# Performance work log

Hardware: AMD Instinct MI355X
Metric: run time of the kernel (lower is better)

## Reference

```python
import jax, jax.numpy as jnp
import numpy as np

B, N, D = 8, 2048, 512  # batch, input_dim (tokens), weight_dim


def setup_inputs() -> dict:
    key = jax.random.key(0)
    ks = jax.random.split(key, 7)
    return {
        "query": jax.random.normal(ks[0], (B, N, D), dtype=jnp.float32),
        "key": jax.random.normal(ks[1], (B, N, D), dtype=jnp.float32),
        "value": jax.random.normal(ks[2], (B, N, D), dtype=jnp.float32),
        "W_query": jax.random.normal(ks[3], (D, D), dtype=jnp.float32),
        "W_key": jax.random.normal(ks[4], (D, D), dtype=jnp.float32),
        "W_value": jax.random.normal(ks[5], (D, D), dtype=jnp.float32),
        "self_importance": jnp.zeros((N,), dtype=jnp.float32),
    }


def reference(query, key, value, W_query, W_key, W_value, self_importance):
    d = W_query.shape[0]
    q = jnp.einsum("bnd,de->bne", query, W_query)
    k = jnp.einsum("bnd,de->bne", key, W_key)
    v = jnp.einsum("bnd,de->bne", value, W_value)
    scores = jnp.einsum("bqe,bke->bqk", q, k) / jnp.sqrt(jnp.float32(d))
    # diagonal self-importance bias: eye(N) * clamp(exp(s), max=3)
    importance = jnp.minimum(jnp.exp(self_importance), 3.0)  # [N]
    n = scores.shape[1]
    idx = jnp.arange(n)
    scores = scores.at[:, idx, idx].add(importance)
    attn = jax.nn.softmax(scores, axis=-1)  # [B, N, N]
    entropy_loss = -jnp.mean(jnp.sum(attn * jnp.log(attn + 1e-10), axis=-1))
    out = jnp.einsum("bqk,bke->bqe", attn, v)
    return (out, attn, entropy_loss)
```

## Files before the change

### kernel.cpp

```cpp
#include <hip/hip_runtime.h>
#include <math.h>

#define BB 8
#define NN 2048
#define DD 512

typedef _Float16 halfT;
typedef _Float16 half8 __attribute__((ext_vector_type(8)));
typedef _Float16 half4 __attribute__((ext_vector_type(4)));
typedef float f32x4 __attribute__((ext_vector_type(4)));

#define GLOAD16(gp, sp) __builtin_amdgcn_global_load_lds( \
    (const __attribute__((address_space(1))) void*)(gp), \
    (__attribute__((address_space(3))) void*)(sp), 16, 0, 0)

__global__ __launch_bounds__(256) void wsplit_kernel(
    const float* __restrict__ Wq, const float* __restrict__ Wk, const float* __restrict__ Wv,
    _Float16* __restrict__ qhT, _Float16* __restrict__ qlT,
    _Float16* __restrict__ khT, _Float16* __restrict__ klT,
    _Float16* __restrict__ vhT)
{
    __shared__ float t[64][65];
    const int z = blockIdx.z;
    const float* W = (z == 0) ? Wq : ((z == 1) ? Wk : Wv);
    _Float16* Ph = (z == 0) ? qhT : ((z == 1) ? khT : vhT);
    _Float16* Pl = (z == 0) ? qlT : ((z == 1) ? klT : nullptr);
    const int bx = blockIdx.x * 64, by = blockIdx.y * 64;
    const int tid = threadIdx.x;
    #pragma unroll
    for (int i = 0; i < 16; ++i) {
        const int idx = i * 256 + tid;
        const int r = idx >> 6, c = idx & 63;
        t[r][c] = W[(long)(by + r) * 512 + bx + c];
    }
    __syncthreads();
    #pragma unroll
    for (int i = 0; i < 16; ++i) {
        const int idx = i * 256 + tid;
        const int r = idx >> 6, c = idx & 63;
        const float v = t[c][r];
        const _Float16 h = (_Float16)v;
        const long o = (long)(bx + r) * 512 + by + c;
        Ph[o] = h;
        if (z < 2) Pl[o] = (_Float16)(v - (float)h);
    }
}

__global__ __launch_bounds__(512, 2) void proj_kernel(
    const float* __restrict__ X0, const float* __restrict__ X1, const float* __restrict__ X2,
    const halfT* __restrict__ B0h, const halfT* __restrict__ B0l,
    const halfT* __restrict__ B1h, const halfT* __restrict__ B1l,
    const halfT* __restrict__ B2h,
    halfT* __restrict__ O0h, halfT* __restrict__ O0l,
    halfT* __restrict__ O1h, halfT* __restrict__ O1l,
    halfT* __restrict__ O2)
{
    extern __shared__ __align__(16) char smem[];

    const int tid  = threadIdx.x;
    const int lane = tid & 63;
    const int w    = tid >> 6;
    const int wr   = w >> 1, wc = w & 1;

    const int h = blockIdx.x;
    int z, nx, my;
    if (h < 512) {
        const int L = ((h & 7) << 6) | (h >> 3);
        z = L >> 8; nx = L & 3; my = (L >> 2) & 63;
    } else {
        const int hv = h - 512;
        const int L = ((hv & 7) << 5) | (hv >> 3);
        z = 2; nx = L & 3; my = L >> 2;
    }
    const int bm = my * 256, bn = nx * 128;
    const bool full = (z < 2);

    const float* X = (z == 0) ? X0 : ((z == 1) ? X1 : X2);
    const halfT* Bgh = (z == 0) ? B0h : ((z == 1) ? B1h : B2h);
    const halfT* Bgl = (z == 0) ? B0l : B1l;
    halfT* Oh = (z == 0) ? O0h : O1h;
    halfT* Ol = (z == 0) ? O0l : O1l;

    const int b_row   = w * 16 + (lane >> 2);
    const int b_chunk = (lane & 3) ^ ((lane >> 3) & 3);
    const long gB = (long)(bn + b_row) * DD + b_chunk * 8;
    const int ldstB = w * 1024;

    const int a_row0 = tid >> 2;
    const int a_gc   = tid & 3;
    const int a_phys = a_gc ^ ((a_row0 >> 1) & 3);
    const long gA0 = (long)(bm + a_row0) * DD + a_gc * 8;
    const long gA1 = (long)(bm + a_row0 + 128) * DD + a_gc * 8;
    const int aOff0 = a_row0 * 64 + a_phys * 16;
    const int aOff1 = (a_row0 + 128) * 64 + a_phys * 16;

    float ar[16];
    auto loadA = [&](int t) {
        const long kk = (long)t * 32;
        *(float4*)&ar[0]  = *(const float4*)(X + gA0 + kk);
        *(float4*)&ar[4]  = *(const float4*)(X + gA0 + kk + 4);
        *(float4*)&ar[8]  = *(const float4*)(X + gA1 + kk);
        *(float4*)&ar[12] = *(const float4*)(X + gA1 + kk + 4);
    };
    auto stageB = [&](char* buf, int t) {
        const long kk = (long)t * 32;
        GLOAD16(Bgh + gB + kk, buf + 32768 + ldstB);
        if (full) GLOAD16(Bgl + gB + kk, buf + 40960 + ldstB);
    };
    auto writeA = [&](char* buf) {
        half8 h0, l0, h1, l1;
        #pragma unroll
        for (int i = 0; i < 8; ++i) {
            const _Float16 hh = (_Float16)ar[i];
            h0[i] = hh; l0[i] = (_Float16)(ar[i] - (float)hh);
        }
        #pragma unroll
        for (int i = 0; i < 8; ++i) {
            const _Float16 hh = (_Float16)ar[8 + i];
            h1[i] = hh; l1[i] = (_Float16)(ar[8 + i] - (float)hh);
        }
        *(half8*)(buf + aOff0) = h0;
        *(half8*)(buf + aOff1) = h1;
        if (full) {
            *(half8*)(buf + 16384 + aOff0) = l0;
            *(half8*)(buf + 16384 + aOff1) = l1;
        }
    };

    const int lr  = lane & 15;
    const int q16 = lane >> 4;
    const int frag = lr * 64 + ((q16 ^ ((lr >> 1) & 3)) << 4);
    const int abase = wr * 4096 + frag;
    const int bbase = wc * 4096 + frag;

    f32x4 acc[4][4];
    #pragma unroll
    for (int i = 0; i < 4; ++i)
        #pragma unroll
        for (int j = 0; j < 4; ++j) acc[i][j] = (f32x4)0.0f;

    loadA(0);
    stageB(smem, 0);
    writeA(smem);
    asm volatile("s_waitcnt vmcnt(0) lgkmcnt(0)" ::: "memory");
    __builtin_amdgcn_s_barrier();
    __builtin_amdgcn_sched_barrier(0);

    for (int t = 0; t < 16; ++t) {
        char* cur = smem + (size_t)(t & 1) * 49152;
        char* nxt = smem + (size_t)((t + 1) & 1) * 49152;
        const bool pf = (t < 15);

        if (pf) { loadA(t + 1); stageB(nxt, t + 1); }

        half8 ah[4], bh[4], bl[4];
        #pragma unroll
        for (int m = 0; m < 4; ++m)
            ah[m] = *(const half8*)(cur + abase + m * 1024);
        #pragma unroll
        for (int j = 0; j < 4; ++j)
            bh[j] = *(const half8*)(cur + 32768 + bbase + j * 1024);
        __builtin_amdgcn_s_setprio(1);
        #pragma unroll
        for (int m = 0; m < 4; ++m)
            #pragma unroll
            for (int j = 0; j < 4; ++j)
                acc[m][j] = __builtin_amdgcn_mfma_f32_16x16x32_f16(ah[m], bh[j], acc[m][j], 0, 0, 0);
        __builtin_amdgcn_s_setprio(0);

        if (full) {
            #pragma unroll
            for (int j = 0; j < 4; ++j)
                bl[j] = *(const half8*)(cur + 40960 + bbase + j * 1024);
            __builtin_amdgcn_s_setprio(1);
            #pragma unroll
            for (int m = 0; m < 4; ++m)
                #pragma unroll
                for (int j = 0; j < 4; ++j)
                    acc[m][j] = __builtin_amdgcn_mfma_f32_16x16x32_f16(ah[m], bl[j], acc[m][j], 0, 0, 0);
            __builtin_amdgcn_s_setprio(0);

            __builtin_amdgcn_s_setprio(1);
            #pragma unroll
            for (int m = 0; m < 4; ++m) {
                const half8 al = *(const half8*)(cur + 16384 + abase + m * 1024);
                #pragma unroll
                for (int j = 0; j < 4; ++j)
                    acc[m][j] = __builtin_amdgcn_mfma_f32_16x16x32_f16(al, bh[j], acc[m][j], 0, 0, 0);
            }
            __builtin_amdgcn_s_setprio(0);
        }

        if (pf) writeA(nxt);
        asm volatile("s_waitcnt vmcnt(0) lgkmcnt(0)" ::: "memory");
        __builtin_amdgcn_s_barrier();
        __builtin_amdgcn_sched_barrier(0);
    }

    if (full) {
        #pragma unroll
        for (int m = 0; m < 4; ++m) {
            const int rb = bm + wr * 64 + m * 16 + (q16 << 2);
            #pragma unroll
            for (int j = 0; j < 4; ++j) {
                const int gc = bn + wc * 64 + j * 16 + lr;
                #pragma unroll
                for (int r = 0; r < 4; ++r) {
                    const float vv = acc[m][j][r];
                    const _Float16 hh = (_Float16)vv;
                    const long o = (long)(rb + r) * DD + gc;
                    Oh[o] = hh;
                    Ol[o] = (_Float16)(vv - (float)hh);
                }
            }
        }
    } else {
        #pragma unroll
        for (int m = 0; m < 4; ++m) {
            const int rb = bm + wr * 64 + m * 16 + (q16 << 2);
            #pragma unroll
            for (int j = 0; j < 4; ++j) {
                const int gc = bn + wc * 64 + j * 16 + lr;
                half4 hv;
                #pragma unroll
                for (int r = 0; r < 4; ++r) hv[r] = (_Float16)acc[m][j][r];
                const int b = rb >> 11, rIn = rb & 2047;
                *(half4*)&O2[((long)b * 512 + gc) * 2048 + rIn] = hv;
            }
        }
    }
}

__global__ __launch_bounds__(512, 2) void scores256_kernel(
    const halfT* __restrict__ qh, const halfT* __restrict__ ql,
    const halfT* __restrict__ kh, const halfT* __restrict__ kl,
    float* __restrict__ C, const float* __restrict__ si, float scale)
{
    extern __shared__ __align__(16) char smem[];

    const int tid  = threadIdx.x;
    const int lane = tid & 63;
    const int w    = tid >> 6;
    const int wr   = w >> 2, wc = w & 3;

    int flat = (blockIdx.z << 6) | (blockIdx.y << 3) | blockIdx.x;
    flat = ((flat & 7) << 6) | (flat >> 3);
    const int bx = flat & 7, by = (flat >> 3) & 7, bz = flat >> 6;
    const int bm = by * 256, bn = bx * 256;

    const long zoff = (long)bz * NN * DD;
    const halfT* A_h = qh + zoff;
    const halfT* A_l = ql + zoff;
    const halfT* B_h = kh + zoff;
    const halfT* B_l = kl + zoff;

    const int s_row   = w * 16 + (lane >> 2);
    const int s_chunk = (lane & 3) ^ ((lane >> 3) & 3);
    const long gA = (long)(bm + s_row) * DD + s_chunk * 8;
    const long gB = (long)(bn + s_row) * DD + s_chunk * 8;
    const int ldst = w * 1024;
    const long rstep = (long)128 * DD;

    auto stage = [&](char* buf, int t) {
        const long kk = (long)t * 32;
        GLOAD16(A_h + gA + kk,         buf + ldst);
        GLOAD16(A_h + gA + rstep + kk, buf + 8192 + ldst);
        GLOAD16(A_l + gA + kk,         buf + 16384 + ldst);
        GLOAD16(A_l + gA + rstep + kk, buf + 16384 + 8192 + ldst);
        GLOAD16(B_h + gB + kk,         buf + 32768 + ldst);
        GLOAD16(B_h + gB + rstep + kk, buf + 32768 + 8192 + ldst);
        GLOAD16(B_l + gB + kk,         buf + 49152 + ldst);
        GLOAD16(B_l + gB + rstep + kk, buf + 49152 + 8192 + ldst);
    };

    const int lr   = lane & 15;
    const int q16  = lane >> 4;
    const int fswz = (lr >> 1) & 3;
    const int frag = lr * 64 + ((q16 ^ fswz) << 4);
    const int abase = wr * 8192 + frag;
    const int bbase = wc * 4096 + frag;

    f32x4 acc[8][4];
    #pragma unroll
    for (int m = 0; m < 8; ++m)
        #pragma unroll
        for (int n = 0; n < 4; ++n) acc[m][n] = (f32x4)0.0f;

    stage(smem, 0);
    asm volatile("s_waitcnt vmcnt(0)" ::: "memory");
    __builtin_amdgcn_s_barrier();

    for (int t = 0; t < 16; ++t) {
        char* cur = smem + (size_t)(t & 1) * 65536;
        char* nxt = smem + (size_t)((t + 1) & 1) * 65536;

        if (t < 15) stage(nxt, t + 1);

        half8 ah[8], bh[4], bl[4];
        #pragma unroll
        for (int n = 0; n < 4; ++n)
            bh[n] = *(const half8*)(cur + 32768 + bbase + n * 1024);
        #pragma unroll
        for (int m = 0; m < 8; ++m)
            ah[m] = *(const half8*)(cur + abase + m * 1024);
        __builtin_amdgcn_s_setprio(1);
        #pragma unroll
        for (int m = 0; m < 8; ++m)
            #pragma unroll
            for (int n = 0; n < 4; ++n)
                acc[m][n] = __builtin_amdgcn_mfma_f32_16x16x32_f16(ah[m], bh[n], acc[m][n], 0, 0, 0);
        __builtin_amdgcn_s_setprio(0);

        #pragma unroll
        for (int n = 0; n < 4; ++n)
            bl[n] = *(const half8*)(cur + 49152 + bbase + n * 1024);
        __builtin_amdgcn_s_setprio(1);
        #pragma unroll
        for (int m = 0; m < 8; ++m)
            #pragma unroll
            for (int n = 0; n < 4; ++n)
                acc[m][n] = __builtin_amdgcn_mfma_f32_16x16x32_f16(ah[m], bl[n], acc[m][n], 0, 0, 0);
        __builtin_amdgcn_s_setprio(0);

        __builtin_amdgcn_s_setprio(1);
        #pragma unroll
        for (int m = 0; m < 8; ++m) {
            const half8 al = *(const half8*)(cur + 16384 + abase + m * 1024);
            #pragma unroll
            for (int n = 0; n < 4; ++n)
                acc[m][n] = __builtin_amdgcn_mfma_f32_16x16x32_f16(al, bh[n], acc[m][n], 0, 0, 0);
        }
        __builtin_amdgcn_s_setprio(0);

        if (t < 15) {
            asm volatile("s_waitcnt vmcnt(0)" ::: "memory");
            __builtin_amdgcn_s_barrier();
        }
    }

    float* Cz = C + (long)bz * NN * NN;
    #pragma unroll
    for (int m = 0; m < 8; ++m) {
        const int rb = bm + wr * 128 + m * 16 + ((lane >> 4) << 2);
        #pragma unroll
        for (int n = 0; n < 4; ++n) {
            const int gc = bn + wc * 64 + n * 16 + (lane & 15);
            #pragma unroll
            for (int r = 0; r < 4; ++r) {
                const int gr = rb + r;
                float vv = acc[m][n][r] * scale;
                if (gr == gc) vv += fminf(expf(si[gr]), 3.0f);
                Cz[(long)gr * NN + gc] = vv;
            }
        }
    }
}

__global__ __launch_bounds__(512, 2) void av_kernel(
    const halfT* __restrict__ P, const halfT* __restrict__ V,
    float* __restrict__ O)
{
    extern __shared__ __align__(16) char smem[];

    const int tid  = threadIdx.x;
    const int lane = tid & 63;
    const int w    = tid >> 6;
    const int wr   = w >> 1, wc = w & 1;

    int flat = blockIdx.x;
    flat = ((flat & 7) << 5) | (flat >> 3);
    const int nx = flat & 3, my = (flat >> 2) & 7, bz = flat >> 5;
    const int bm = my * 256, bn = nx * 128;

    const halfT* A = P + (long)bz * NN * NN;
    const halfT* B = V + (long)bz * DD * NN;

    const int s_row   = w * 16 + (lane >> 2);
    const int s_chunk = (lane & 3) ^ ((lane >> 3) & 3);
    const long gA = (long)(bm + s_row) * NN + s_chunk * 8;
    const long gB = (long)(bn + s_row) * NN + s_chunk * 8;
    const int ldst = w * 1024;
    const long rstep = (long)128 * NN;

    auto stage = [&](char* buf, int t) {
        const long kk = (long)t * 32;
        GLOAD16(A + gA + kk,         buf + ldst);
        GLOAD16(A + gA + rstep + kk, buf + 8192 + ldst);
        GLOAD16(B + gB + kk,         buf + 16384 + ldst);
    };

    const int lr  = lane & 15;
    const int q16 = lane >> 4;
    const int frag = lr * 64 + ((q16 ^ ((lr >> 1) & 3)) << 4);
    const int abase = wr * 4096 + frag;
    const int bbase = wc * 4096 + frag;

    f32x4 acc[4][4];
    #pragma unroll
    for (int m = 0; m < 4; ++m)
        #pragma unroll
        for (int j = 0; j < 4; ++j) acc[m][j] = (f32x4)0.0f;

    stage(smem, 0);
    stage(smem + 24576, 1);
    asm volatile("s_waitcnt vmcnt(3)" ::: "memory");
    __builtin_amdgcn_s_barrier();
    __builtin_amdgcn_sched_barrier(0);

    int cb = 0;
    for (int t = 0; t < 64; ++t) {
        char* cur = smem + (size_t)cb * 24576;
        const int nb = (cb + 2 >= 3) ? cb - 1 : cb + 2;
        if (t < 62) stage(smem + (size_t)nb * 24576, t + 2);

        half8 ah[4], bh[4];
        #pragma unroll
        for (int m = 0; m < 4; ++m)
            ah[m] = *(const half8*)(cur + abase + m * 1024);
        #pragma unroll
        for (int j = 0; j < 4; ++j)
            bh[j] = *(const half8*)(cur + 16384 + bbase + j * 1024);
        __builtin_amdgcn_s_setprio(1);
        #pragma unroll
        for (int m = 0; m < 4; ++m)
            #pragma unroll
            for (int j = 0; j < 4; ++j)
                acc[m][j] = __builtin_amdgcn_mfma_f32_16x16x32_f16(ah[m], bh[j], acc[m][j], 0, 0, 0);
        __builtin_amdgcn_s_setprio(0);

        if (t < 63) {
            if (t < 62) { asm volatile("s_waitcnt vmcnt(3)" ::: "memory"); }
            else        { asm volatile("s_waitcnt vmcnt(0)" ::: "memory"); }
            __builtin_amdgcn_s_barrier();
            __builtin_amdgcn_sched_barrier(0);
        }
        cb = (cb + 1 == 3) ? 0 : cb + 1;
    }

    float* Oz = O + (long)bz * NN * DD;
    #pragma unroll
    for (int m = 0; m < 4; ++m) {
        const int rb = bm + wr * 64 + m * 16 + (q16 << 2);
        #pragma unroll
        for (int j = 0; j < 4; ++j) {
            const int gc = bn + wc * 64 + j * 16 + lr;
            #pragma unroll
            for (int r = 0; r < 4; ++r)
                Oz[(long)(rb + r) * DD + gc] = acc[m][j][r];
        }
    }
}

__global__ __launch_bounds__(256) void softmax_entropy_kernel(
    float* __restrict__ attn, _Float16* __restrict__ ah, float* __restrict__ partials)
{
    __shared__ float red[4];
    const long row = blockIdx.x;
    float* p = attn + row * (long)NN;
    _Float16* ph = ah + row * (long)NN;
    const int tid = threadIdx.x;
    const int base = tid * 8;

    float4 va = *(const float4*)(p + base);
    float4 vb = *(const float4*)(p + base + 4);
    float v[8] = {va.x, va.y, va.z, va.w, vb.x, vb.y, vb.z, vb.w};

    float m = v[0];
    #pragma unroll
    for (int i = 1; i < 8; ++i) m = fmaxf(m, v[i]);
    #pragma unroll
    for (int o = 32; o; o >>= 1) m = fmaxf(m, __shfl_xor(m, o, 64));
    if ((tid & 63) == 0) red[tid >> 6] = m;
    __syncthreads();
    m = fmaxf(fmaxf(red[0], red[1]), fmaxf(red[2], red[3]));

    float t[8];
    float s = 0.f;
    #pragma unroll
    for (int i = 0; i < 8; ++i) { t[i] = v[i] - m; v[i] = expf(t[i]); s += v[i]; }
    #pragma unroll
    for (int o = 32; o; o >>= 1) s += __shfl_xor(s, o, 64);
    __syncthreads();
    if ((tid & 63) == 0) red[tid >> 6] = s;
    __syncthreads();
    s = red[0] + red[1] + red[2] + red[3];

    const float inv = 1.0f / s;
    const float lns = logf(s);
    float e = 0.f;
    float pv[8];
    #pragma unroll
    for (int i = 0; i < 8; ++i) {
        pv[i] = v[i] * inv;
        e = fmaf(pv[i], t[i] - lns, e);
    }
    *(float4*)(p + base)     = make_float4(pv[0], pv[1], pv[2], pv[3]);
    *(float4*)(p + base + 4) = make_float4(pv[4], pv[5], pv[6], pv[7]);
    half8 h;
    #pragma unroll
    for (int i = 0; i < 8; ++i) h[i] = (_Float16)pv[i];
    *(half8*)(ph + base) = h;

    #pragma unroll
    for (int o = 32; o; o >>= 1) e += __shfl_xor(e, o, 64);
    __syncthreads();
    if ((tid & 63) == 0) red[tid >> 6] = e;
    __syncthreads();
    if (tid == 0) partials[row] = red[0] + red[1] + red[2] + red[3];
}

__global__ __launch_bounds__(256) void ent_reduce_kernel(
    const float* __restrict__ partials, float* __restrict__ ent)
{
    __shared__ float red[4];
    float s = 0.f;
    for (int i = threadIdx.x; i < BB * NN; i += 256) s += partials[i];
    #pragma unroll
    for (int o = 32; o; o >>= 1) s += __shfl_xor(s, o, 64);
    if ((threadIdx.x & 63) == 0) red[threadIdx.x >> 6] = s;
    __syncthreads();
    if (threadIdx.x == 0)
        *ent = -(red[0] + red[1] + red[2] + red[3]) / (float)(BB * NN);
}

extern "C" void kernel_launch(void* const* d_in, const int* in_sizes, int n_in,
                              void* d_out, int out_size, void* d_ws, size_t ws_size,
                              hipStream_t stream) {
    const float* query = (const float*)d_in[0];
    const float* key   = (const float*)d_in[1];
    const float* value = (const float*)d_in[2];
    const float* Wq    = (const float*)d_in[3];
    const float* Wk    = (const float*)d_in[4];
    const float* Wv    = (const float*)d_in[5];
    const float* si    = (const float*)d_in[6];

    float* out  = (float*)d_out;
    float* attn = out + (size_t)BB * NN * DD;
    float* ent  = attn + (size_t)BB * NN * NN;

    const size_t NK = (size_t)BB * NN * DD;
    _Float16* ws16 = (_Float16*)d_ws;
    _Float16* qh = ws16;
    _Float16* ql = qh + NK;
    _Float16* kh = ql + NK;
    _Float16* kl = kh + NK;
    _Float16* vT = kl + NK;
    _Float16* WqhT = vT + NK;
    _Float16* WqlT = WqhT + DD * DD;
    _Float16* WkhT = WqlT + DD * DD;
    _Float16* WklT = WkhT + DD * DD;
    _Float16* WvhT = WklT + DD * DD;
    float* partials = (float*)(WvhT + DD * DD);
    _Float16* attn_h = ws16;

    const dim3 blk(256);
    const float inv_sqrt_d = 0.044194173824159216f;

    wsplit_kernel<<<dim3(8, 8, 3), blk, 0, stream>>>(Wq, Wk, Wv,
        WqhT, WqlT, WkhT, WklT, WvhT);

    proj_kernel<<<dim3(768), dim3(512), 98304, stream>>>(
        query, key, value, WqhT, WqlT, WkhT, WklT, WvhT,
        qh, ql, kh, kl, vT);

    scores256_kernel<<<dim3(8, 8, 8), dim3(512), 131072, stream>>>(
        qh, ql, kh, kl, attn, si, inv_sqrt_d);

    softmax_entropy_kernel<<<dim3(BB * NN), blk, 0, stream>>>(attn, attn_h, partials);
    ent_reduce_kernel<<<dim3(1), blk, 0, stream>>>(partials, ent);

    av_kernel<<<dim3(256), dim3(512), 73728, stream>>>(attn_h, vT, out);
}
```

Before: 293.5 us.

## Feed fp32 attention straight into AV kernel, converting to fp16 in registers

The softmax kernel no longer writes a separate fp16 copy of the attention matrix. The AV GEMM now reads the fp32 attention directly through registers, converts it to fp16 and stores it into swizzled LDS, while V is still loaded via global_load_lds. This removes one full write pass of the fp16 attention buffer. In exchange, the AV kernel reads twice as many bytes for A, drops from triple to double buffering, and waits on vmcnt(0) every iteration, which may reduce latency hiding.

```diff
diff --git a/kernel.cpp b/kernel.cpp
--- a/kernel.cpp
+++ b/kernel.cpp
@@ -357,7 +357,7 @@
 }
 
 __global__ __launch_bounds__(512, 2) void av_kernel(
-    const halfT* __restrict__ P, const halfT* __restrict__ V,
+    const float* __restrict__ P, const halfT* __restrict__ V,
     float* __restrict__ O)
 {
     extern __shared__ __align__(16) char smem[];
@@ -372,21 +372,41 @@
     const int nx = flat & 3, my = (flat >> 2) & 7, bz = flat >> 5;
     const int bm = my * 256, bn = nx * 128;
 
-    const halfT* A = P + (long)bz * NN * NN;
+    const float* A = P + (long)bz * NN * NN;
     const halfT* B = V + (long)bz * DD * NN;
 
-    const int s_row   = w * 16 + (lane >> 2);
-    const int s_chunk = (lane & 3) ^ ((lane >> 3) & 3);
-    const long gA = (long)(bm + s_row) * NN + s_chunk * 8;
-    const long gB = (long)(bn + s_row) * NN + s_chunk * 8;
-    const int ldst = w * 1024;
-    const long rstep = (long)128 * NN;
-
-    auto stage = [&](char* buf, int t) {
+    const int a_row0 = tid >> 2;
+    const int a_gc   = tid & 3;
+    const int a_phys = a_gc ^ ((a_row0 >> 1) & 3);
+    const long gA0 = (long)(bm + a_row0) * NN + a_gc * 8;
+    const long gA1 = (long)(bm + a_row0 + 128) * NN + a_gc * 8;
+    const int aOff0 = a_row0 * 64 + a_phys * 16;
+    const int aOff1 = (a_row0 + 128) * 64 + a_phys * 16;
+
+    float ar[16];
+    auto loadA = [&](int t) {
         const long kk = (long)t * 32;
-        GLOAD16(A + gA + kk,         buf + ldst);
-        GLOAD16(A + gA + rstep + kk, buf + 8192 + ldst);
-        GLOAD16(B + gB + kk,         buf + 16384 + ldst);
+        *(float4*)&ar[0]  = *(const float4*)(A + gA0 + kk);
+        *(float4*)&ar[4]  = *(const float4*)(A + gA0 + kk + 4);
+        *(float4*)&ar[8]  = *(const float4*)(A + gA1 + kk);
+        *(float4*)&ar[12] = *(const float4*)(A + gA1 + kk + 4);
+    };
+    auto writeA = [&](char* buf) {
+        half8 h0, h1;
+        #pragma unroll
+        for (int i = 0; i < 8; ++i) h0[i] = (_Float16)ar[i];
+        #pragma unroll
+        for (int i = 0; i < 8; ++i) h1[i] = (_Float16)ar[8 + i];
+        *(half8*)(buf + aOff0) = h0;
+        *(half8*)(buf + aOff1) = h1;
+    };
+
+    const int b_row   = w * 16 + (lane >> 2);
+    const int b_chunk = (lane & 3) ^ ((lane >> 3) & 3);
+    const long gB = (long)(bn + b_row) * NN + b_chunk * 8;
+    const int ldstB = w * 1024;
+    auto stageB = [&](char* buf, int t) {
+        GLOAD16(B + gB + (long)t * 32, buf + 16384 + ldstB);
     };
 
     const int lr  = lane & 15;
@@ -401,17 +421,19 @@
         #pragma unroll
         for (int j = 0; j < 4; ++j) acc[m][j] = (f32x4)0.0f;
 
-    stage(smem, 0);
-    stage(smem + 24576, 1);
-    asm volatile("s_waitcnt vmcnt(3)" ::: "memory");
+    loadA(0);
+    stageB(smem, 0);
+    writeA(smem);
+    asm volatile("s_waitcnt vmcnt(0) lgkmcnt(0)" ::: "memory");
     __builtin_amdgcn_s_barrier();
     __builtin_amdgcn_sched_barrier(0);
 
-    int cb = 0;
     for (int t = 0; t < 64; ++t) {
-        char* cur = smem + (size_t)cb * 24576;
-        const int nb = (cb + 2 >= 3) ? cb - 1 : cb + 2;
-        if (t < 62) stage(smem + (size_t)nb * 24576, t + 2);
+        char* cur = smem + (size_t)(t & 1) * 24576;
+        char* nxt = smem + (size_t)((t + 1) & 1) * 24576;
+        const bool pf = (t < 63);
+
+        if (pf) { loadA(t + 1); stageB(nxt, t + 1); }
 
         half8 ah[4], bh[4];
         #pragma unroll
@@ -428,13 +450,10 @@
                 acc[m][j] = __builtin_amdgcn_mfma_f32_16x16x32_f16(ah[m], bh[j], acc[m][j], 0, 0, 0);
         __builtin_amdgcn_s_setprio(0);
 
-        if (t < 63) {
-            if (t < 62) { asm volatile("s_waitcnt vmcnt(3)" ::: "memory"); }
-            else        { asm volatile("s_waitcnt vmcnt(0)" ::: "memory"); }
-            __builtin_amdgcn_s_barrier();
-            __builtin_amdgcn_sched_barrier(0);
-        }
-        cb = (cb + 1 == 3) ? 0 : cb + 1;
+        if (pf) writeA(nxt);
+        asm volatile("s_waitcnt vmcnt(0) lgkmcnt(0)" ::: "memory");
+        __builtin_amdgcn_s_barrier();
+        __builtin_amdgcn_sched_barrier(0);
     }
 
     float* Oz = O + (long)bz * NN * DD;
@@ -452,12 +471,11 @@
 }
 
 __global__ __launch_bounds__(256) void softmax_entropy_kernel(
-    float* __restrict__ attn, _Float16* __restrict__ ah, float* __restrict__ partials)
+    float* __restrict__ attn, float* __restrict__ partials)
 {
     __shared__ float red[4];
     const long row = blockIdx.x;
     float* p = attn + row * (long)NN;
-    _Float16* ph = ah + row * (long)NN;
     const int tid = threadIdx.x;
     const int base = tid * 8;
 
@@ -496,10 +514,6 @@
     }
     *(float4*)(p + base)     = make_float4(pv[0], pv[1], pv[2], pv[3]);
     *(float4*)(p + base + 4) = make_float4(pv[4], pv[5], pv[6], pv[7]);
-    half8 h;
-    #pragma unroll
-    for (int i = 0; i < 8; ++i) h[i] = (_Float16)pv[i];
-    *(half8*)(ph + base) = h;
 
     #pragma unroll
     for (int o = 32; o; o >>= 1) e += __shfl_xor(e, o, 64);
@@ -551,7 +565,6 @@
     _Float16* WklT = WkhT + DD * DD;
     _Float16* WvhT = WklT + DD * DD;
     float* partials = (float*)(WvhT + DD * DD);
-    _Float16* attn_h = ws16;
 
     const dim3 blk(256);
     const float inv_sqrt_d = 0.044194173824159216f;
@@ -566,8 +579,8 @@
     scores256_kernel<<<dim3(8, 8, 8), dim3(512), 131072, stream>>>(
         qh, ql, kh, kl, attn, si, inv_sqrt_d);
 
-    softmax_entropy_kernel<<<dim3(BB * NN), blk, 0, stream>>>(attn, attn_h, partials);
+    softmax_entropy_kernel<<<dim3(BB * NN), blk, 0, stream>>>(attn, partials);
     ent_reduce_kernel<<<dim3(1), blk, 0, stream>>>(partials, ent);
 
-    av_kernel<<<dim3(256), dim3(512), 73728, stream>>>(attn_h, vT, out);
-}
+    av_kernel<<<dim3(256), dim3(512), 49152, stream>>>(attn, vT, out);
+}
```

New measurement: 303.6 us. 3.4% more time.

## Shrink projection tiles to 128x128 with 256 threads and single-buffered static LDS

Applied to the files above, without the earlier changes.

The projection GEMM moves from 512-thread blocks on 256x128 tiles with 96KB double-buffered dynamic LDS to 256-thread blocks on 128x128 tiles with a 32KB single static buffer. The grid doubles to 1536 blocks with a new block-index swizzle, and the software pipeline is replaced by a simpler write, sync, compute, sync loop. The goal is higher occupancy and more blocks per CU to hide latency. The cost is lost overlap between global loads and MFMA work, plus lower per-block data reuse.

```diff
diff --git a/kernel.cpp b/kernel.cpp
--- a/kernel.cpp
+++ b/kernel.cpp
@@ -46,7 +46,7 @@
     }
 }
 
-__global__ __launch_bounds__(512, 2) void proj_kernel(
+__global__ __launch_bounds__(256) void proj_kernel(
     const float* __restrict__ X0, const float* __restrict__ X1, const float* __restrict__ X2,
     const halfT* __restrict__ B0h, const halfT* __restrict__ B0l,
     const halfT* __restrict__ B1h, const halfT* __restrict__ B1l,
@@ -55,24 +55,19 @@
     halfT* __restrict__ O1h, halfT* __restrict__ O1l,
     halfT* __restrict__ O2)
 {
-    extern __shared__ __align__(16) char smem[];
+    __shared__ __align__(16) char smem[32768];
 
     const int tid  = threadIdx.x;
     const int lane = tid & 63;
     const int w    = tid >> 6;
     const int wr   = w >> 1, wc = w & 1;
 
-    const int h = blockIdx.x;
+    int h = blockIdx.x;
+    h = (h & 7) * 192 + (h >> 3);
     int z, nx, my;
-    if (h < 512) {
-        const int L = ((h & 7) << 6) | (h >> 3);
-        z = L >> 8; nx = L & 3; my = (L >> 2) & 63;
-    } else {
-        const int hv = h - 512;
-        const int L = ((hv & 7) << 5) | (hv >> 3);
-        z = 2; nx = L & 3; my = L >> 2;
-    }
-    const int bm = my * 256, bn = nx * 128;
+    if (h < 1024) { z = h >> 9; const int r = h & 511; nx = r & 3; my = r >> 2; }
+    else          { const int r = h - 1024; z = 2;     nx = r & 3; my = r >> 2; }
+    const int bm = my * 128, bn = nx * 128;
     const bool full = (z < 2);
 
     const float* X = (z == 0) ? X0 : ((z == 1) ? X1 : X2);
@@ -83,47 +78,51 @@
 
     const int b_row   = w * 16 + (lane >> 2);
     const int b_chunk = (lane & 3) ^ ((lane >> 3) & 3);
-    const long gB = (long)(bn + b_row) * DD + b_chunk * 8;
+    const long gB0 = (long)(bn + b_row) * DD + b_chunk * 8;
+    const long gB1 = (long)(bn + b_row + 64) * DD + b_chunk * 8;
     const int ldstB = w * 1024;
 
-    const int a_row0 = tid >> 2;
-    const int a_gc   = tid & 3;
-    const int a_phys = a_gc ^ ((a_row0 >> 1) & 3);
-    const long gA0 = (long)(bm + a_row0) * DD + a_gc * 8;
-    const long gA1 = (long)(bm + a_row0 + 128) * DD + a_gc * 8;
-    const int aOff0 = a_row0 * 64 + a_phys * 16;
-    const int aOff1 = (a_row0 + 128) * 64 + a_phys * 16;
+    const int a_row = tid >> 1;
+    const int g0    = (tid & 1) << 1;
+    const int aswz  = (a_row >> 1) & 3;
+    const int p0 = g0 ^ aswz, p1 = (g0 + 1) ^ aswz;
+    const long gA = (long)(bm + a_row) * DD + g0 * 8;
+    const int aOff0 = a_row * 64 + p0 * 16;
+    const int aOff1 = a_row * 64 + p1 * 16;
 
     float ar[16];
     auto loadA = [&](int t) {
         const long kk = (long)t * 32;
-        *(float4*)&ar[0]  = *(const float4*)(X + gA0 + kk);
-        *(float4*)&ar[4]  = *(const float4*)(X + gA0 + kk + 4);
-        *(float4*)&ar[8]  = *(const float4*)(X + gA1 + kk);
-        *(float4*)&ar[12] = *(const float4*)(X + gA1 + kk + 4);
+        *(float4*)&ar[0]  = *(const float4*)(X + gA + kk);
+        *(float4*)&ar[4]  = *(const float4*)(X + gA + kk + 4);
+        *(float4*)&ar[8]  = *(const float4*)(X + gA + kk + 8);
+        *(float4*)&ar[12] = *(const float4*)(X + gA + kk + 12);
     };
-    auto stageB = [&](char* buf, int t) {
+    auto stageB = [&](int t) {
         const long kk = (long)t * 32;
-        GLOAD16(Bgh + gB + kk, buf + 32768 + ldstB);
-        if (full) GLOAD16(Bgl + gB + kk, buf + 40960 + ldstB);
+        GLOAD16(Bgh + gB0 + kk, smem + 16384 + ldstB);
+        GLOAD16(Bgh + gB1 + kk, smem + 16384 + 4096 + ldstB);
+        if (full) {
+            GLOAD16(Bgl + gB0 + kk, smem + 24576 + ldstB);
+            GLOAD16(Bgl + gB1 + kk, smem + 24576 + 4096 + ldstB);
+        }
     };
-    auto writeA = [&](char* buf) {
-        half8 h0, l0, h1, l1;
-        #pragma unroll
-        for (int i = 0; i < 8; ++i) {
-            const _Float16 hh = (_Float16)ar[i];
-            h0[i] = hh; l0[i] = (_Float16)(ar[i] - (float)hh);
-        }
-        #pragma unroll
-        for (int i = 0; i < 8; ++i) {
-            const _Float16 hh = (_Float16)ar[8 + i];
-            h1[i] = hh; l1[i] = (_Float16)(ar[8 + i] - (float)hh);
-        }
-        *(half8*)(buf + aOff0) = h0;
-        *(half8*)(buf + aOff1) = h1;
+    auto writeA = [&]() {
+        half8 h0, h1;
+        #pragma unroll
+        for (int i = 0; i < 8; ++i) h0[i] = (_Float16)ar[i];
+        #pragma unroll
+        for (int i = 0; i < 8; ++i) h1[i] = (_Float16)ar[8 + i];
+        *(half8*)(smem + aOff0) = h0;
+        *(half8*)(smem + aOff1) = h1;
         if (full) {
-            *(half8*)(buf + 16384 + aOff0) = l0;
-            *(half8*)(buf + 16384 + aOff1) = l1;
+            half8 l0, l1;
+            #pragma unroll
+            for (int i = 0; i < 8; ++i) l0[i] = (_Float16)(ar[i] - (float)h0[i]);
+            #pragma unroll
+            for (int i = 0; i < 8; ++i) l1[i] = (_Float16)(ar[8 + i] - (float)h1[i]);
+            *(half8*)(smem + 8192 + aOff0) = l0;
+            *(half8*)(smem + 8192 + aOff1) = l1;
         }
     };
 
@@ -140,26 +139,20 @@
         for (int j = 0; j < 4; ++j) acc[i][j] = (f32x4)0.0f;
 
     loadA(0);
-    stageB(smem, 0);
-    writeA(smem);
-    asm volatile("s_waitcnt vmcnt(0) lgkmcnt(0)" ::: "memory");
-    __builtin_amdgcn_s_barrier();
-    __builtin_amdgcn_sched_barrier(0);
 
     for (int t = 0; t < 16; ++t) {
-        char* cur = smem + (size_t)(t & 1) * 49152;
-        char* nxt = smem + (size_t)((t + 1) & 1) * 49152;
-        const bool pf = (t < 15);
-
-        if (pf) { loadA(t + 1); stageB(nxt, t + 1); }
-
-        half8 ah[4], bh[4], bl[4];
+        writeA();
+        stageB(t);
+        if (t < 15) loadA(t + 1);
+        __syncthreads();
+
+        half8 ah[4], bh[4];
         #pragma unroll
         for (int m = 0; m < 4; ++m)
-            ah[m] = *(const half8*)(cur + abase + m * 1024);
+            ah[m] = *(const half8*)(smem + abase + m * 1024);
         #pragma unroll
         for (int j = 0; j < 4; ++j)
-            bh[j] = *(const half8*)(cur + 32768 + bbase + j * 1024);
+            bh[j] = *(const half8*)(smem + 16384 + bbase + j * 1024);
         __builtin_amdgcn_s_setprio(1);
         #pragma unroll
         for (int m = 0; m < 4; ++m)
@@ -169,9 +162,10 @@
         __builtin_amdgcn_s_setprio(0);
 
         if (full) {
+            half8 bl[4];
             #pragma unroll
             for (int j = 0; j < 4; ++j)
-                bl[j] = *(const half8*)(cur + 40960 + bbase + j * 1024);
+                bl[j] = *(const half8*)(smem + 24576 + bbase + j * 1024);
             __builtin_amdgcn_s_setprio(1);
             #pragma unroll
             for (int m = 0; m < 4; ++m)
@@ -183,18 +177,14 @@
             __builtin_amdgcn_s_setprio(1);
             #pragma unroll
             for (int m = 0; m < 4; ++m) {
-                const half8 al = *(const half8*)(cur + 16384 + abase + m * 1024);
+                const half8 al = *(const half8*)(smem + 8192 + abase + m * 1024);
                 #pragma unroll
                 for (int j = 0; j < 4; ++j)
                     acc[m][j] = __builtin_amdgcn_mfma_f32_16x16x32_f16(al, bh[j], acc[m][j], 0, 0, 0);
             }
             __builtin_amdgcn_s_setprio(0);
         }
-
-        if (pf) writeA(nxt);
-        asm volatile("s_waitcnt vmcnt(0) lgkmcnt(0)" ::: "memory");
-        __builtin_amdgcn_s_barrier();
-        __builtin_amdgcn_sched_barrier(0);
+        __syncthreads();
     }
 
     if (full) {
@@ -559,7 +549,7 @@
     wsplit_kernel<<<dim3(8, 8, 3), blk, 0, stream>>>(Wq, Wk, Wv,
         WqhT, WqlT, WkhT, WklT, WvhT);
 
-    proj_kernel<<<dim3(768), dim3(512), 98304, stream>>>(
+    proj_kernel<<<dim3(1536), blk, 0, stream>>>(
         query, key, value, WqhT, WqlT, WkhT, WklT, WvhT,
         qh, ql, kh, kl, vT);
 
```

Result: slower. 302.2 us (+3.0%).
